# Optimization experiments

Hardware: AMD Instinct MI355X
Metric: run time of the kernel (lower is better)

## Reference

```python
import jax, jax.numpy as jnp
import numpy as np

# Dims forced/chosen per module code: n_embd=256 hardcoded via torch.split(x, 256, dim=2)
B, S, E, H, D, L, V, NI = 4, 2048, 256, 8, 32, 2, 50257, 1024
EPS = 1e-5
MASK_VALUE = -10000.0
INIT_STD = 0.02


def _layernorm(x, g, b):
    mu = jnp.mean(x, axis=-1, keepdims=True)
    var = jnp.var(x, axis=-1, keepdims=True)
    return (x - mu) * jax.lax.rsqrt(var + EPS) * g + b


def setup_inputs() -> dict:
    key = jax.random.key(0)
    ks = jax.random.split(key, 8)
    s = INIT_STD
    return {
        "input_ids": jax.random.randint(ks[0], (B, S), 0, V),
        "wte": jax.random.normal(ks[1], (V, E), dtype=jnp.float32) * s,
        "wpe": jax.random.normal(ks[2], (S, E), dtype=jnp.float32) * s,
        # per-layer params stacked on leading L axis (for lax.scan)
        "ln1_g": jnp.ones((L, E)), "ln1_b": jnp.zeros((L, E)),
        "qkv_w": jax.random.normal(ks[3], (L, E, 3 * E), dtype=jnp.float32) * s,
        "qkv_b": jnp.zeros((L, 3 * E)),
        "proj_w": jax.random.normal(ks[4], (L, E, E), dtype=jnp.float32) * s,
        "proj_b": jnp.zeros((L, E)),
        "ln2_g": jnp.ones((L, E)), "ln2_b": jnp.zeros((L, E)),
        "fc1_w": jax.random.normal(ks[5], (L, E, NI), dtype=jnp.float32) * s,
        "fc1_b": jnp.zeros((L, NI)),
        "fc2_w": jax.random.normal(ks[6], (L, NI, E), dtype=jnp.float32) * s,
        "fc2_b": jnp.zeros((L, E)),
        "lnf_g": jnp.ones((E,)), "lnf_b": jnp.zeros((E,)),
    }


def _forward(input_ids, wte, wpe, ln1_g, ln1_b, qkv_w, qkv_b, proj_w, proj_b,
             ln2_g, ln2_b, fc1_w, fc1_b, fc2_w, fc2_b, lnf_g, lnf_b):
    h = wte[input_ids] + wpe[jnp.arange(S)]  # [B,S,E]; embd dropout p=0 -> identity
    causal = jnp.tril(jnp.ones((S, S), dtype=bool))  # built each call, as in source
    scale = jnp.asarray(1.0 / np.sqrt(D), dtype=h.dtype)

    def block(h, p):
        g1, b1, Wqkv, bqkv, Wp, bp, g2, b2, W1, b1m, W2, b2m = p
        x = _layernorm(h, g1, b1)
        qkv = x @ Wqkv + bqkv                     # [B,S,3E]
        q, k, v = jnp.split(qkv, 3, axis=-1)      # torch.split(x, 256, dim=2)
        heads = lambda t: t.reshape(B, S, H, D).transpose(0, 2, 1, 3)  # [B,H,S,D]
        q, k, v = heads(q), heads(k), heads(v)
        scores = jnp.einsum('bhqd,bhkd->bhqk', q, k) * scale
        scores = jnp.where(causal, scores, MASK_VALUE)  # masked_fill with -10000.0
        probs = jax.nn.softmax(scores, axis=-1)         # attn dropout p=0 -> identity
        out = jnp.einsum('bhqk,bhkd->bhqd', probs, v)
        out = out.transpose(0, 2, 1, 3).reshape(B, S, E)
        h = h + (out @ Wp + bp)                   # resid dropout p=0 -> identity
        x2 = _layernorm(h, g2, b2)
        m = jax.nn.gelu(x2 @ W1 + b1m, approximate=True) @ W2 + b2m  # gelu_new (tanh)
        return h + m, None

    h, _ = jax.lax.scan(block, h, (ln1_g, ln1_b, qkv_w, qkv_b, proj_w, proj_b,
                                   ln2_g, ln2_b, fc1_w, fc1_b, fc2_w, fc2_b))
    return _layernorm(h, lnf_g, lnf_b)


def reference(input_ids, wte, wpe, ln1_g, ln1_b, qkv_w, qkv_b, proj_w, proj_b,
              ln2_g, ln2_b, fc1_w, fc1_b, fc2_w, fc2_b, lnf_g, lnf_b):
    return _forward(input_ids, wte, wpe, ln1_g, ln1_b, qkv_w, qkv_b, proj_w,
                    proj_b, ln2_g, ln2_b, fc1_w, fc1_b, fc2_w, fc2_b, lnf_g, lnf_b)
```

## Files before the change

kernel.cpp:

```cpp
#include <hip/hip_runtime.h>
#include <hip/hip_bf16.h>
#include <math.h>

#define BB 4
#define SS 2048
#define EE 256
#define HH 8
#define DD 32
#define LL 2
#define NI 1024
#define NROWS (BB*SS)
#define NRL   (BB*HH*SS)

typedef float f32x4 __attribute__((ext_vector_type(4)));
typedef short s16x8 __attribute__((ext_vector_type(8)));
typedef __bf16 bf16x8 __attribute__((ext_vector_type(8)));
typedef unsigned short ushort_t;

#define QSCALE 0.2550352699458294f

__device__ __forceinline__ unsigned short f2bf(float f) {
    return __builtin_bit_cast(unsigned short, (__bf16)f);
}
__device__ __forceinline__ float bf2f(unsigned short s) {
    return __uint_as_float((unsigned)s << 16);
}
__device__ __forceinline__ f32x4 mfma16x16x32(s16x8 a, s16x8 b, f32x4 c) {
    return __builtin_amdgcn_mfma_f32_16x16x32_bf16(
        __builtin_bit_cast(bf16x8, a), __builtin_bit_cast(bf16x8, b), c, 0, 0, 0);
}

__global__ __launch_bounds__(256) void embed_ln_kernel(
    const int* __restrict__ ids, const float* __restrict__ wte,
    const float* __restrict__ wpe, const float* __restrict__ g,
    const float* __restrict__ b, float* __restrict__ h, ushort_t* __restrict__ x)
{
    int row  = blockIdx.x * 4 + (threadIdx.x >> 6);
    int s    = row & (SS - 1);
    int lane = threadIdx.x & 63;
    int id   = ids[row];
    float4 a = *(const float4*)(wte + (size_t)id * EE + lane * 4);
    float4 p = *(const float4*)(wpe + (size_t)s  * EE + lane * 4);
    float4 v = { a.x + p.x, a.y + p.y, a.z + p.z, a.w + p.w };
    *(float4*)(h + (size_t)row * EE + lane * 4) = v;
    float sm  = v.x + v.y + v.z + v.w;
    float ss2 = v.x*v.x + v.y*v.y + v.z*v.z + v.w*v.w;
    #pragma unroll
    for (int off = 32; off; off >>= 1) {
        sm  += __shfl_xor(sm,  off);
        ss2 += __shfl_xor(ss2, off);
    }
    float mu  = sm * (1.f / EE);
    float var = ss2 * (1.f / EE) - mu * mu;
    float rs  = rsqrtf(var + 1e-5f);
    float4 gv = *(const float4*)(g + lane * 4);
    float4 bv = *(const float4*)(b + lane * 4);
    ushort4 w = { f2bf((v.x - mu) * rs * gv.x + bv.x),
                  f2bf((v.y - mu) * rs * gv.y + bv.y),
                  f2bf((v.z - mu) * rs * gv.z + bv.z),
                  f2bf((v.w - mu) * rs * gv.w + bv.w) };
    *(ushort4*)(x + (size_t)row * EE + lane * 4) = w;
}

template<bool OUTBF>
__global__ __launch_bounds__(256) void ln_kernel(
    const float* __restrict__ in, const float* __restrict__ g,
    const float* __restrict__ b, void* __restrict__ out)
{
    int row  = blockIdx.x * 4 + (threadIdx.x >> 6);
    int lane = threadIdx.x & 63;
    float4 v = *(const float4*)(in + (size_t)row * EE + lane * 4);
    float s  = v.x + v.y + v.z + v.w;
    float ss = v.x*v.x + v.y*v.y + v.z*v.z + v.w*v.w;
    #pragma unroll
    for (int off = 32; off; off >>= 1) {
        s  += __shfl_xor(s,  off);
        ss += __shfl_xor(ss, off);
    }
    float mu  = s * (1.f / EE);
    float var = ss * (1.f / EE) - mu * mu;
    float rs  = rsqrtf(var + 1e-5f);
    float4 gv = *(const float4*)(g + lane * 4);
    float4 bv = *(const float4*)(b + lane * 4);
    float4 o;
    o.x = (v.x - mu) * rs * gv.x + bv.x;
    o.y = (v.y - mu) * rs * gv.y + bv.y;
    o.z = (v.z - mu) * rs * gv.z + bv.z;
    o.w = (v.w - mu) * rs * gv.w + bv.w;
    if (OUTBF) {
        ushort4 w = { f2bf(o.x), f2bf(o.y), f2bf(o.z), f2bf(o.w) };
        *(ushort4*)((ushort_t*)out + (size_t)row * EE + lane * 4) = w;
    } else {
        *(float4*)((float*)out + (size_t)row * EE + lane * 4) = o;
    }
}

__global__ __launch_bounds__(256) void wconv_all(
    const float* __restrict__ qkv_w, const float* __restrict__ proj_w,
    const float* __restrict__ fc1_w, const float* __restrict__ fc2_w,
    ushort_t* __restrict__ wq_t, ushort_t* __restrict__ wp_t,
    ushort_t* __restrict__ w1_t, ushort_t* __restrict__ w2_t)
{
    __shared__ float t_[32][33];
    int l = blockIdx.y, t = blockIdx.x;
    const float* W; ushort_t* Wt; int K, N, n0, k0;
    if (t < 192)      { W = qkv_w  + (size_t)l*EE*3*EE; Wt = wq_t + (size_t)l*3*EE*EE;
                        K = EE; N = 3*EE; int u = t;       n0 = (u % 24) * 32; k0 = (u / 24) * 32; }
    else if (t < 256) { W = proj_w + (size_t)l*EE*EE;   Wt = wp_t + (size_t)l*EE*EE;
                        K = EE; N = EE;   int u = t - 192; n0 = (u % 8)  * 32; k0 = (u / 8)  * 32; }
    else if (t < 512) { W = fc1_w  + (size_t)l*EE*NI;   Wt = w1_t + (size_t)l*EE*NI;
                        K = EE; N = NI;   int u = t - 256; n0 = (u % 32) * 32; k0 = (u / 32) * 32; }
    else              { W = fc2_w  + (size_t)l*NI*EE;   Wt = w2_t + (size_t)l*NI*EE;
                        K = NI; N = EE;   int u = t - 512; n0 = (u % 8)  * 32; k0 = (u / 8)  * 32; }
    int tx = threadIdx.x & 31, ty = threadIdx.x >> 5;
    #pragma unroll
    for (int i = 0; i < 4; ++i) {
        int k = ty + i * 8;
        t_[k][tx] = W[(size_t)(k0 + k) * N + n0 + tx];
    }
    __syncthreads();
    #pragma unroll
    for (int i = 0; i < 4; ++i) {
        int n = ty + i * 8;
        Wt[(size_t)(n0 + n) * K + k0 + tx] = f2bf(t_[tx][n]);
    }
}

template<int MI, bool OUT_BF, bool GELU_ACT, bool RES, bool QSC>
__global__ __launch_bounds__(256) void gemm_bf(
    const ushort_t* __restrict__ A, const ushort_t* __restrict__ Bt,
    const float* __restrict__ bias, const float* __restrict__ res,
    void* __restrict__ C, int M, int N, int K)
{
    __shared__ __align__(16) ushort_t As[MI*64][40];
    __shared__ __align__(16) ushort_t Bs[64][40];
    int tid = threadIdx.x;
    int wid = tid >> 6, lane = tid & 63;
    int h = lane >> 4, c = lane & 15;

    int nbx = gridDim.x;
    int nwg = nbx * gridDim.y;
    int flat = blockIdx.y * nbx + blockIdx.x;
    int v = (flat & 7) * (nwg >> 3) + (flat >> 3);
    int bx = v % nbx, by = v / nbx;

    f32x4 acc[MI][4] = {};

    int arow = tid >> 2, ac = tid & 3;
    const ushort_t* Ap = A  + (size_t)(by * (MI*64) + arow) * K + ac * 8;
    const ushort_t* Bp = Bt + (size_t)(bx * 64     + arow) * K + ac * 8;

    s16x8 a0[MI], a1[MI], b0, b1;
    #pragma unroll
    for (int i = 0; i < MI; ++i) a0[i] = *(const s16x8*)(Ap + (size_t)i * 64 * K);
    b0 = *(const s16x8*)(Bp);
    #pragma unroll
    for (int i = 0; i < MI; ++i) a1[i] = *(const s16x8*)(Ap + (size_t)i * 64 * K + 32);
    b1 = *(const s16x8*)(Bp + 32);

    for (int k0 = 0; k0 < K; k0 += 64) {
        asm volatile("s_waitcnt lgkmcnt(0)" ::: "memory");
        __builtin_amdgcn_s_barrier();
        asm volatile("" ::: "memory");
        #pragma unroll
        for (int i = 0; i < MI; ++i)
            *(s16x8*)&As[i * 64 + arow][ac * 8] = a0[i];
        *(s16x8*)&Bs[arow][ac * 8] = b0;
        if (k0 + 64 < K) {
            #pragma unroll
            for (int i = 0; i < MI; ++i)
                a0[i] = *(const s16x8*)(Ap + (size_t)i * 64 * K + k0 + 64);
            b0 = *(const s16x8*)(Bp + k0 + 64);
        }
        asm volatile("s_waitcnt lgkmcnt(0)" ::: "memory");
        __builtin_amdgcn_s_barrier();
        asm volatile("" ::: "memory");
        {
            s16x8 af[MI], bfr[4];
            #pragma unroll
            for (int i = 0; i < MI; ++i)
                af[i] = *(const s16x8*)&As[wid * (MI*16) + i * 16 + c][h * 8];
            #pragma unroll
            for (int j = 0; j < 4; ++j)
                bfr[j] = *(const s16x8*)&Bs[j * 16 + c][h * 8];
            #pragma unroll
            for (int i = 0; i < MI; ++i)
                #pragma unroll
                for (int j = 0; j < 4; ++j)
                    acc[i][j] = mfma16x16x32(af[i], bfr[j], acc[i][j]);
        }
        asm volatile("s_waitcnt lgkmcnt(0)" ::: "memory");
        __builtin_amdgcn_s_barrier();
        asm volatile("" ::: "memory");
        #pragma unroll
        for (int i = 0; i < MI; ++i)
            *(s16x8*)&As[i * 64 + arow][ac * 8] = a1[i];
        *(s16x8*)&Bs[arow][ac * 8] = b1;
        if (k0 + 96 < K) {
            #pragma unroll
            for (int i = 0; i < MI; ++i)
                a1[i] = *(const s16x8*)(Ap + (size_t)i * 64 * K + k0 + 96);
            b1 = *(const s16x8*)(Bp + k0 + 96);
        }
        asm volatile("s_waitcnt lgkmcnt(0)" ::: "memory");
        __builtin_amdgcn_s_barrier();
        asm volatile("" ::: "memory");
        {
            s16x8 af[MI], bfr[4];
            #pragma unroll
            for (int i = 0; i < MI; ++i)
                af[i] = *(const s16x8*)&As[wid * (MI*16) + i * 16 + c][h * 8];
            #pragma unroll
            for (int j = 0; j < 4; ++j)
                bfr[j] = *(const s16x8*)&Bs[j * 16 + c][h * 8];
            #pragma unroll
            for (int i = 0; i < MI; ++i)
                #pragma unroll
                for (int j = 0; j < 4; ++j)
                    acc[i][j] = mfma16x16x32(af[i], bfr[j], acc[i][j]);
        }
    }

    float bj[4];
    #pragma unroll
    for (int j = 0; j < 4; ++j) bj[j] = bias[bx * 64 + j * 16 + c];
    #pragma unroll
    for (int i = 0; i < MI; ++i) {
        #pragma unroll
        for (int r = 0; r < 4; ++r) {
            int row = by * (MI*64) + wid * (MI*16) + i * 16 + h * 4 + r;
            #pragma unroll
            for (int j = 0; j < 4; ++j) {
                int col = bx * 64 + j * 16 + c;
                float v2 = acc[i][j][r] + bj[j];
                if (QSC && col < EE) v2 *= QSCALE;
                if (RES) v2 += res[(size_t)row * N + col];
                if (GELU_ACT) {
                    float t = v2;
                    v2 = 0.5f * t * (1.f + tanhf(0.7978845608028654f *
                                                 (t + 0.044715f * t * t * t)));
                }
                if (OUT_BF) ((ushort_t*)C)[(size_t)row * N + col] = f2bf(v2);
                else        ((float*)C)[(size_t)row * N + col]    = v2;
            }
        }
    }
}

#define QB 64
#define KSTR 40
#define VSTR 88
#define PSTR 72
#define PTILES 8
__global__ __launch_bounds__(256) void attn_kernel(
    const ushort_t* __restrict__ qkv, ushort_t* __restrict__ o_part,
    float* __restrict__ l_part, ushort_t* __restrict__ attno)
{
    __shared__ __align__(16) ushort_t Ks[QB][KSTR];
    __shared__ __align__(16) ushort_t Vt[DD][VSTR];
    __shared__ __align__(16) ushort_t Ps[4][16][PSTR];

    int tid  = threadIdx.x;
    int p    = 79 - blockIdx.x;
    int qt, ks;
    if (p < 8)       { qt = p;                 ks = 0; }
    else if (p < 24) { qt = 8  + ((p-8)  >> 1); ks = (p-8)  & 1; }
    else if (p < 48) { qt = 16 + (p-24) / 3;    ks = (p-24) % 3; }
    else             { qt = 24 + ((p-48) >> 2); ks = (p-48) & 3; }
    int hh   = blockIdx.y, b = blockIdx.z;
    int wid  = tid >> 6, lane = tid & 63;
    int h    = lane >> 4, c = lane & 15;

    int qfrow = qt * QB + wid * 16 + c;
    s16x8 qfrag = *(const s16x8*)(qkv + ((size_t)(b * SS + qfrow)) * (3*EE)
                                  + hh * DD + h * 8);

    s16x8 onesf = { (short)0x3F80, (short)0x3F80, (short)0x3F80, (short)0x3F80,
                    (short)0x3F80, (short)0x3F80, (short)0x3F80, (short)0x3F80 };

    f32x4 o0 = {0.f,0.f,0.f,0.f}, o1 = {0.f,0.f,0.f,0.f}, o2 = {0.f,0.f,0.f,0.f};

    int srow = tid >> 2, scq = tid & 3;
    int t0 = ks * PTILES;
    int t1 = min(t0 + PTILES, qt + 1);

    s16x8 kreg, vreg;
    {
        const ushort_t* kb = qkv + ((size_t)(b * SS + t0 * QB)) * (3*EE) + hh * DD + EE;
        kreg = *(const s16x8*)(kb + (size_t)srow * (3*EE) + scq * 8);
        vreg = *(const s16x8*)(kb + EE + (size_t)srow * (3*EE) + scq * 8);
    }

    for (int kt = t0; kt < t1; ++kt) {
        int k0 = kt * QB;

        __syncthreads();

        *(s16x8*)&Ks[srow][scq * 8] = kreg;
        {
            int d0 = scq * 8;
            int colw = srow ^ (scq << 4);
            #pragma unroll
            for (int j = 0; j < 8; ++j) Vt[d0 + j][colw] = (ushort_t)vreg[j];
        }
        if (kt + 1 < t1) {
            const ushort_t* kb2 = qkv + ((size_t)(b * SS + (kt+1) * QB)) * (3*EE)
                                  + hh * DD + EE;
            kreg = *(const s16x8*)(kb2 + (size_t)srow * (3*EE) + scq * 8);
            vreg = *(const s16x8*)(kb2 + EE + (size_t)srow * (3*EE) + scq * 8);
        }

        asm volatile("s_waitcnt lgkmcnt(0)" ::: "memory");
        __builtin_amdgcn_s_barrier();
        asm volatile("" ::: "memory");

        __builtin_amdgcn_s_setprio(1);

        f32x4 sg[4];
        #pragma unroll
        for (int g = 0; g < 4; ++g) {
            s16x8 kf = *(const s16x8*)&Ks[g * 16 + c][h * 8];
            f32x4 z = {0.f,0.f,0.f,0.f};
            sg[g] = mfma16x16x32(kf, qfrag, z);
        }

        bool diag = (kt == qt);
        int klim = qfrow - k0;

        #pragma unroll
        for (int g = 0; g < 4; ++g) {
            ushort4 pk;
            #pragma unroll
            for (int r = 0; r < 4; ++r) {
                float x = sg[g][r];
                if (diag && (g * 16 + h * 4 + r > klim)) x = -INFINITY;
                ((ushort_t*)&pk)[r] = f2bf(exp2f(x));
            }
            *(ushort4*)&Ps[wid][c][g * 16 + h * 4] = pk;
        }

        #pragma unroll
        for (int kc = 0; kc < 2; ++kc) {
            int kbase = kc * 32 + h * 8;
            s16x8 pf = *(const s16x8*)&Ps[wid][c][kbase];
            s16x8 v0 = *(const s16x8*)&Vt[c]     [kbase ^ ((c >> 3) << 4)];
            s16x8 v1 = *(const s16x8*)&Vt[16 + c][kbase ^ (((16 + c) >> 3) << 4)];
            o0 = mfma16x16x32(pf, v0, o0);
            o1 = mfma16x16x32(pf, v1, o1);
            o2 = mfma16x16x32(pf, onesf, o2);
        }

        __builtin_amdgcn_s_setprio(0);
    }

    if (qt < PTILES) {
        #pragma unroll
        for (int r = 0; r < 4; ++r) {
            int qrow = qt * QB + wid * 16 + h * 4 + r;
            float inv = 1.f / o2[r];
            ushort_t* ap = attno + ((size_t)(b * SS + qrow)) * EE + hh * DD;
            ap[c]      = f2bf(o0[r] * inv);
            ap[16 + c] = f2bf(o1[r] * inv);
        }
    } else {
        size_t rbase = (size_t)(b * HH + hh) * SS;
        #pragma unroll
        for (int r = 0; r < 4; ++r) {
            int qrow = qt * QB + wid * 16 + h * 4 + r;
            size_t rl = rbase + qrow;
            ushort_t* op = o_part + ((size_t)ks * NRL + rl) * DD;
            op[c]      = f2bf(o0[r]);
            op[16 + c] = f2bf(o1[r]);
            if (c == 0) l_part[(size_t)ks * NRL + rl] = o2[r];
        }
    }
}

__global__ __launch_bounds__(256) void attn_merge(
    const ushort_t* __restrict__ o_part, const float* __restrict__ l_part,
    ushort_t* __restrict__ attno)
{
    int g = blockIdx.x * 256 + threadIdx.x;
    int rl = g >> 3;
    int d0 = (g & 7) * 4;
    int srow = rl & (SS - 1);
    int qt = srow >> 6;
    if (qt < PTILES) return;
    int np = (qt >> 3) + 1;

    float acc0 = 0.f, acc1 = 0.f, acc2 = 0.f, acc3 = 0.f, L = 0.f;
    #pragma unroll
    for (int i = 0; i < 4; ++i) {
        if (i < np) {
            L += l_part[(size_t)i * NRL + rl];
            ushort4 ov = *(const ushort4*)(o_part + ((size_t)i * NRL + rl) * DD + d0);
            acc0 += bf2f(ov.x); acc1 += bf2f(ov.y);
            acc2 += bf2f(ov.z); acc3 += bf2f(ov.w);
        }
    }
    float inv = 1.f / L;
    int b  = rl >> 14;
    int hh = (rl >> 11) & 7;
    ushort4 w4 = { f2bf(acc0*inv), f2bf(acc1*inv), f2bf(acc2*inv), f2bf(acc3*inv) };
    *(ushort4*)(attno + ((size_t)(b * SS + srow)) * EE + hh * DD + d0) = w4;
}

extern "C" void kernel_launch(void* const* d_in, const int* in_sizes, int n_in,
                              void* d_out, int out_size, void* d_ws, size_t ws_size,
                              hipStream_t stream)
{
    const int*   ids    = (const int*)  d_in[0];
    const float* wte    = (const float*)d_in[1];
    const float* wpe    = (const float*)d_in[2];
    const float* ln1_g  = (const float*)d_in[3];
    const float* ln1_b  = (const float*)d_in[4];
    const float* qkv_w  = (const float*)d_in[5];
    const float* qkv_b  = (const float*)d_in[6];
    const float* proj_w = (const float*)d_in[7];
    const float* proj_b = (const float*)d_in[8];
    const float* ln2_g  = (const float*)d_in[9];
    const float* ln2_b  = (const float*)d_in[10];
    const float* fc1_w  = (const float*)d_in[11];
    const float* fc1_b  = (const float*)d_in[12];
    const float* fc2_w  = (const float*)d_in[13];
    const float* fc2_b  = (const float*)d_in[14];
    const float* lnf_g  = (const float*)d_in[15];
    const float* lnf_b  = (const float*)d_in[16];

    float*    h        = (float*)d_ws;
    ushort_t* x_bf     = (ushort_t*)(h + (size_t)NROWS*EE);
    ushort_t* qkv_bf   = x_bf   + (size_t)NROWS*EE;
    ushort_t* attno_bf = qkv_bf + (size_t)NROWS*3*EE;
    ushort_t* m1_bf    = attno_bf + (size_t)NROWS*EE;
    ushort_t* wq_t     = m1_bf  + (size_t)NROWS*NI;
    ushort_t* wp_t     = wq_t   + (size_t)2*3*EE*EE;
    ushort_t* w1_t     = wp_t   + (size_t)2*EE*EE;
    ushort_t* w2_t     = w1_t   + (size_t)2*EE*NI;

    ushort_t* o_part   = m1_bf;
    float*    l_part   = (float*)x_bf;

    wconv_all<<<dim3(768, LL), 256, 0, stream>>>(
        qkv_w, proj_w, fc1_w, fc2_w, wq_t, wp_t, w1_t, w2_t);

    embed_ln_kernel<<<NROWS/4, 256, 0, stream>>>(ids, wte, wpe, ln1_g, ln1_b, h, x_bf);

    for (int l = 0; l < LL; ++l) {
        if (l > 0)
            ln_kernel<true><<<NROWS/4, 256, 0, stream>>>(h, ln1_g + l*EE, ln1_b + l*EE, x_bf);
        gemm_bf<2,true,false,false,true><<<dim3(3*EE/64, NROWS/128), 256, 0, stream>>>(
            x_bf, wq_t + (size_t)l*3*EE*EE, qkv_b + (size_t)l*3*EE, nullptr,
            qkv_bf, NROWS, 3*EE, EE);
        attn_kernel<<<dim3(80, HH, BB), 256, 0, stream>>>(qkv_bf, o_part, l_part, attno_bf);
        attn_merge<<<NRL*8/256, 256, 0, stream>>>(o_part, l_part, attno_bf);
        gemm_bf<1,false,false,true,false><<<dim3(EE/64, NROWS/64), 256, 0, stream>>>(
            attno_bf, wp_t + (size_t)l*EE*EE, proj_b + (size_t)l*EE, h,
            h, NROWS, EE, EE);
        ln_kernel<true><<<NROWS/4, 256, 0, stream>>>(h, ln2_g + l*EE, ln2_b + l*EE, x_bf);
        gemm_bf<2,true,true,false,false><<<dim3(NI/64, NROWS/128), 256, 0, stream>>>(
            x_bf, w1_t + (size_t)l*EE*NI, fc1_b + (size_t)l*NI, nullptr,
            m1_bf, NROWS, NI, EE);
        gemm_bf<1,false,false,true,false><<<dim3(EE/64, NROWS/64), 256, 0, stream>>>(
            m1_bf, w2_t + (size_t)l*NI*EE, fc2_b + (size_t)l*EE, h,
            h, NROWS, EE, NI);
    }

    ln_kernel<false><<<NROWS/4, 256, 0, stream>>>(h, lnf_g, lnf_b, (float*)d_out);
}
```

Baseline: 195.4 us.

## Fuse split-KV attention merge into projection GEMM A-load, cheaper GELU

Removes the separate attn_merge kernel. The attention kernel now always writes partial outputs and row sums, and the projection GEMM reads and combines those partials on the fly while loading its A tile. GELU's tanh is rewritten with exp2 and a reciprocal, and the diagonal mask branch in attention is hoisted out of the inner loop. The cost is that every proj GEMM block reads up to four partials per element, and the first query tiles go through the partial-buffer path instead of writing directly.

```diff
diff --git a/kernel.cpp b/kernel.cpp
--- a/kernel.cpp
+++ b/kernel.cpp
@@ -126,11 +126,12 @@
     }
 }
 
-template<int MI, bool OUT_BF, bool GELU_ACT, bool RES, bool QSC>
+template<int MI, bool OUT_BF, bool GELU_ACT, bool RES, bool QSC, bool MERGEA>
 __global__ __launch_bounds__(256) void gemm_bf(
     const ushort_t* __restrict__ A, const ushort_t* __restrict__ Bt,
     const float* __restrict__ bias, const float* __restrict__ res,
-    void* __restrict__ C, int M, int N, int K)
+    void* __restrict__ C, const float* __restrict__ lp,
+    int M, int N, int K)
 {
     __shared__ __align__(16) ushort_t As[MI*64][40];
     __shared__ __align__(16) ushort_t Bs[64][40];
@@ -150,26 +151,72 @@
     const ushort_t* Ap = A  + (size_t)(by * (MI*64) + arow) * K + ac * 8;
     const ushort_t* Bp = Bt + (size_t)(bx * 64     + arow) * K + ac * 8;
 
+    int mb = 0, msr = 0, mnp = 0, colbase = ac * 8;
+    if (MERGEA) {
+        int mrow = by * 64 + arow;
+        mb  = mrow >> 11;
+        msr = mrow & (SS - 1);
+        mnp = ((msr >> 6) >> 3) + 1;
+    }
+
     s16x8 a0[MI], a1[MI], b0, b1;
-    #pragma unroll
-    for (int i = 0; i < MI; ++i) a0[i] = *(const s16x8*)(Ap + (size_t)i * 64 * K);
+    s16x8 mo0[4], mo1[4];
+    float ml0[4], ml1[4];
+
+    #define M_ISSUE(kk, MO, ML) do {                                          \
+        int col = (kk) + colbase;                                             \
+        int hh2 = col >> 5, d0 = col & 31;                                    \
+        size_t rl = ((size_t)(mb * HH + hh2)) * SS + msr;                     \
+        _Pragma("unroll")                                                     \
+        for (int i_ = 0; i_ < 4; ++i_) {                                      \
+            if (i_ < mnp) {                                                   \
+                MO[i_] = *(const s16x8*)(A + ((size_t)i_ * NRL + rl) * DD + d0); \
+                ML[i_] = lp[(size_t)i_ * NRL + rl];                           \
+            } else { MO[i_] = (s16x8){0,0,0,0,0,0,0,0}; ML[i_] = 0.f; }       \
+        }                                                                     \
+    } while (0)
+
+    #define M_COMBINE(MO, ML, OUTV) do {                                      \
+        float L_ = ML[0] + ML[1] + ML[2] + ML[3];                             \
+        float inv_ = __builtin_amdgcn_rcpf(L_);                               \
+        _Pragma("unroll")                                                     \
+        for (int e_ = 0; e_ < 8; ++e_) {                                      \
+            float s_ = bf2f((ushort_t)MO[0][e_]) + bf2f((ushort_t)MO[1][e_])  \
+                     + bf2f((ushort_t)MO[2][e_]) + bf2f((ushort_t)MO[3][e_]); \
+            OUTV[e_] = (short)f2bf(s_ * inv_);                                \
+        }                                                                     \
+    } while (0)
+
+    if (MERGEA) { M_ISSUE(0, mo0, ml0); M_ISSUE(32, mo1, ml1); }
+    else {
+        #pragma unroll
+        for (int i = 0; i < MI; ++i) a0[i] = *(const s16x8*)(Ap + (size_t)i * 64 * K);
+        #pragma unroll
+        for (int i = 0; i < MI; ++i) a1[i] = *(const s16x8*)(Ap + (size_t)i * 64 * K + 32);
+    }
     b0 = *(const s16x8*)(Bp);
-    #pragma unroll
-    for (int i = 0; i < MI; ++i) a1[i] = *(const s16x8*)(Ap + (size_t)i * 64 * K + 32);
     b1 = *(const s16x8*)(Bp + 32);
 
     for (int k0 = 0; k0 < K; k0 += 64) {
         asm volatile("s_waitcnt lgkmcnt(0)" ::: "memory");
         __builtin_amdgcn_s_barrier();
         asm volatile("" ::: "memory");
-        #pragma unroll
-        for (int i = 0; i < MI; ++i)
-            *(s16x8*)&As[i * 64 + arow][ac * 8] = a0[i];
+        if (MERGEA) {
+            s16x8 mv; M_COMBINE(mo0, ml0, mv);
+            *(s16x8*)&As[arow][ac * 8] = mv;
+        } else {
+            #pragma unroll
+            for (int i = 0; i < MI; ++i)
+                *(s16x8*)&As[i * 64 + arow][ac * 8] = a0[i];
+        }
         *(s16x8*)&Bs[arow][ac * 8] = b0;
         if (k0 + 64 < K) {
-            #pragma unroll
-            for (int i = 0; i < MI; ++i)
-                a0[i] = *(const s16x8*)(Ap + (size_t)i * 64 * K + k0 + 64);
+            if (MERGEA) M_ISSUE(k0 + 64, mo0, ml0);
+            else {
+                #pragma unroll
+                for (int i = 0; i < MI; ++i)
+                    a0[i] = *(const s16x8*)(Ap + (size_t)i * 64 * K + k0 + 64);
+            }
             b0 = *(const s16x8*)(Bp + k0 + 64);
         }
         asm volatile("s_waitcnt lgkmcnt(0)" ::: "memory");
@@ -192,14 +239,22 @@
         asm volatile("s_waitcnt lgkmcnt(0)" ::: "memory");
         __builtin_amdgcn_s_barrier();
         asm volatile("" ::: "memory");
-        #pragma unroll
-        for (int i = 0; i < MI; ++i)
-            *(s16x8*)&As[i * 64 + arow][ac * 8] = a1[i];
+        if (MERGEA) {
+            s16x8 mv; M_COMBINE(mo1, ml1, mv);
+            *(s16x8*)&As[arow][ac * 8] = mv;
+        } else {
+            #pragma unroll
+            for (int i = 0; i < MI; ++i)
+                *(s16x8*)&As[i * 64 + arow][ac * 8] = a1[i];
+        }
         *(s16x8*)&Bs[arow][ac * 8] = b1;
         if (k0 + 96 < K) {
-            #pragma unroll
-            for (int i = 0; i < MI; ++i)
-                a1[i] = *(const s16x8*)(Ap + (size_t)i * 64 * K + k0 + 96);
+            if (MERGEA) M_ISSUE(k0 + 96, mo1, ml1);
+            else {
+                #pragma unroll
+                for (int i = 0; i < MI; ++i)
+                    a1[i] = *(const s16x8*)(Ap + (size_t)i * 64 * K + k0 + 96);
+            }
             b1 = *(const s16x8*)(Bp + k0 + 96);
         }
         asm volatile("s_waitcnt lgkmcnt(0)" ::: "memory");
@@ -220,6 +275,8 @@
                     acc[i][j] = mfma16x16x32(af[i], bfr[j], acc[i][j]);
         }
     }
+    #undef M_ISSUE
+    #undef M_COMBINE
 
     float bj[4];
     #pragma unroll
@@ -236,9 +293,9 @@
                 if (QSC && col < EE) v2 *= QSCALE;
                 if (RES) v2 += res[(size_t)row * N + col];
                 if (GELU_ACT) {
-                    float t = v2;
-                    v2 = 0.5f * t * (1.f + tanhf(0.7978845608028654f *
-                                                 (t + 0.044715f * t * t * t)));
+                    float u = 0.7978845608028654f * (v2 + 0.044715f * v2 * v2 * v2);
+                    float t = exp2f(2.8853900817779268f * u);
+                    v2 = v2 - v2 * __builtin_amdgcn_rcpf(t + 1.f);
                 }
                 if (OUT_BF) ((ushort_t*)C)[(size_t)row * N + col] = f2bf(v2);
                 else        ((float*)C)[(size_t)row * N + col]    = v2;
@@ -254,7 +311,7 @@
 #define PTILES 8
 __global__ __launch_bounds__(256) void attn_kernel(
     const ushort_t* __restrict__ qkv, ushort_t* __restrict__ o_part,
-    float* __restrict__ l_part, ushort_t* __restrict__ attno)
+    float* __restrict__ l_part)
 {
     __shared__ __align__(16) ushort_t Ks[QB][KSTR];
     __shared__ __align__(16) ushort_t Vt[DD][VSTR];
@@ -324,19 +381,28 @@
             sg[g] = mfma16x16x32(kf, qfrag, z);
         }
 
-        bool diag = (kt == qt);
-        int klim = qfrow - k0;
-
-        #pragma unroll
-        for (int g = 0; g < 4; ++g) {
-            ushort4 pk;
-            #pragma unroll
-            for (int r = 0; r < 4; ++r) {
-                float x = sg[g][r];
-                if (diag && (g * 16 + h * 4 + r > klim)) x = -INFINITY;
-                ((ushort_t*)&pk)[r] = f2bf(exp2f(x));
+        if (kt == qt) {
+            int klim = qfrow - k0;
+            #pragma unroll
+            for (int g = 0; g < 4; ++g) {
+                ushort4 pk;
+                #pragma unroll
+                for (int r = 0; r < 4; ++r) {
+                    float x = sg[g][r];
+                    if (g * 16 + h * 4 + r > klim) x = -INFINITY;
+                    ((ushort_t*)&pk)[r] = f2bf(exp2f(x));
+                }
+                *(ushort4*)&Ps[wid][c][g * 16 + h * 4] = pk;
             }
-            *(ushort4*)&Ps[wid][c][g * 16 + h * 4] = pk;
+        } else {
+            #pragma unroll
+            for (int g = 0; g < 4; ++g) {
+                ushort4 pk;
+                #pragma unroll
+                for (int r = 0; r < 4; ++r)
+                    ((ushort_t*)&pk)[r] = f2bf(exp2f(sg[g][r]));
+                *(ushort4*)&Ps[wid][c][g * 16 + h * 4] = pk;
+            }
         }
 
         #pragma unroll
@@ -353,56 +419,16 @@
         __builtin_amdgcn_s_setprio(0);
     }
 
-    if (qt < PTILES) {
-        #pragma unroll
-        for (int r = 0; r < 4; ++r) {
-            int qrow = qt * QB + wid * 16 + h * 4 + r;
-            float inv = 1.f / o2[r];
-            ushort_t* ap = attno + ((size_t)(b * SS + qrow)) * EE + hh * DD;
-            ap[c]      = f2bf(o0[r] * inv);
-            ap[16 + c] = f2bf(o1[r] * inv);
-        }
-    } else {
-        size_t rbase = (size_t)(b * HH + hh) * SS;
-        #pragma unroll
-        for (int r = 0; r < 4; ++r) {
-            int qrow = qt * QB + wid * 16 + h * 4 + r;
-            size_t rl = rbase + qrow;
-            ushort_t* op = o_part + ((size_t)ks * NRL + rl) * DD;
-            op[c]      = f2bf(o0[r]);
-            op[16 + c] = f2bf(o1[r]);
-            if (c == 0) l_part[(size_t)ks * NRL + rl] = o2[r];
-        }
-    }
-}
-
-__global__ __launch_bounds__(256) void attn_merge(
-    const ushort_t* __restrict__ o_part, const float* __restrict__ l_part,
-    ushort_t* __restrict__ attno)
-{
-    int g = blockIdx.x * 256 + threadIdx.x;
-    int rl = g >> 3;
-    int d0 = (g & 7) * 4;
-    int srow = rl & (SS - 1);
-    int qt = srow >> 6;
-    if (qt < PTILES) return;
-    int np = (qt >> 3) + 1;
-
-    float acc0 = 0.f, acc1 = 0.f, acc2 = 0.f, acc3 = 0.f, L = 0.f;
-    #pragma unroll
-    for (int i = 0; i < 4; ++i) {
-        if (i < np) {
-            L += l_part[(size_t)i * NRL + rl];
-            ushort4 ov = *(const ushort4*)(o_part + ((size_t)i * NRL + rl) * DD + d0);
-            acc0 += bf2f(ov.x); acc1 += bf2f(ov.y);
-            acc2 += bf2f(ov.z); acc3 += bf2f(ov.w);
-        }
-    }
-    float inv = 1.f / L;
-    int b  = rl >> 14;
-    int hh = (rl >> 11) & 7;
-    ushort4 w4 = { f2bf(acc0*inv), f2bf(acc1*inv), f2bf(acc2*inv), f2bf(acc3*inv) };
-    *(ushort4*)(attno + ((size_t)(b * SS + srow)) * EE + hh * DD + d0) = w4;
+    size_t rbase = (size_t)(b * HH + hh) * SS;
+    #pragma unroll
+    for (int r = 0; r < 4; ++r) {
+        int qrow = qt * QB + wid * 16 + h * 4 + r;
+        size_t rl = rbase + qrow;
+        ushort_t* op = o_part + ((size_t)ks * NRL + rl) * DD;
+        op[c]      = f2bf(o0[r]);
+        op[16 + c] = f2bf(o1[r]);
+        if (c == 0) l_part[(size_t)ks * NRL + rl] = o2[r];
+    }
 }
 
 extern "C" void kernel_launch(void* const* d_in, const int* in_sizes, int n_in,
@@ -448,21 +474,20 @@
     for (int l = 0; l < LL; ++l) {
         if (l > 0)
             ln_kernel<true><<<NROWS/4, 256, 0, stream>>>(h, ln1_g + l*EE, ln1_b + l*EE, x_bf);
-        gemm_bf<2,true,false,false,true><<<dim3(3*EE/64, NROWS/128), 256, 0, stream>>>(
+        gemm_bf<2,true,false,false,true,false><<<dim3(3*EE/64, NROWS/128), 256, 0, stream>>>(
             x_bf, wq_t + (size_t)l*3*EE*EE, qkv_b + (size_t)l*3*EE, nullptr,
-            qkv_bf, NROWS, 3*EE, EE);
-        attn_kernel<<<dim3(80, HH, BB), 256, 0, stream>>>(qkv_bf, o_part, l_part, attno_bf);
-        attn_merge<<<NRL*8/256, 256, 0, stream>>>(o_part, l_part, attno_bf);
-        gemm_bf<1,false,false,true,false><<<dim3(EE/64, NROWS/64), 256, 0, stream>>>(
-            attno_bf, wp_t + (size_t)l*EE*EE, proj_b + (size_t)l*EE, h,
-            h, NROWS, EE, EE);
+            qkv_bf, nullptr, NROWS, 3*EE, EE);
+        attn_kernel<<<dim3(80, HH, BB), 256, 0, stream>>>(qkv_bf, o_part, l_part);
+        gemm_bf<1,false,false,true,false,true><<<dim3(EE/64, NROWS/64), 256, 0, stream>>>(
+            o_part, wp_t + (size_t)l*EE*EE, proj_b + (size_t)l*EE, h,
+            h, l_part, NROWS, EE, EE);
         ln_kernel<true><<<NROWS/4, 256, 0, stream>>>(h, ln2_g + l*EE, ln2_b + l*EE, x_bf);
-        gemm_bf<2,true,true,false,false><<<dim3(NI/64, NROWS/128), 256, 0, stream>>>(
+        gemm_bf<2,true,true,false,false,false><<<dim3(NI/64, NROWS/128), 256, 0, stream>>>(
             x_bf, w1_t + (size_t)l*EE*NI, fc1_b + (size_t)l*NI, nullptr,
-            m1_bf, NROWS, NI, EE);
-        gemm_bf<1,false,false,true,false><<<dim3(EE/64, NROWS/64), 256, 0, stream>>>(
+            m1_bf, nullptr, NROWS, NI, EE);
+        gemm_bf<1,false,false,true,false,false><<<dim3(EE/64, NROWS/64), 256, 0, stream>>>(
             m1_bf, w2_t + (size_t)l*NI*EE, fc2_b + (size_t)l*EE, h,
-            h, NROWS, EE, NI);
+            h, nullptr, NROWS, EE, NI);
     }
 
     ln_kernel<false><<<NROWS/4, 256, 0, stream>>>(h, lnf_g, lnf_b, (float*)d_out);
```

New measurement: 183.2 us (median of 2 runs). -6.3%, faster.
